# Kernel tuning notes

Hardware: AMD Instinct MI355X
Metric: run time of the kernel (lower is better)

Reference implementation:

```python
import jax, jax.numpy as jnp
from jax import lax
import numpy as np

EPS = 1e-5  # BatchNorm eps (eval mode, fresh running stats: mean=0, var=1)

N, T, H, C = 16, 512, 64, 64
O, K, E = 64, 9, 256


def setup_inputs() -> dict:
    key = jax.random.key(0)
    ks = jax.random.split(key, 16)
    X = jax.random.normal(ks[0], (N, T, H, C), dtype=jnp.float32)
    edges = jax.random.randint(ks[1], (N, 2, E), 0, H, dtype=jnp.int64)
    # att1/att2: Conv2d(C,1,1) == dot over channels + bias
    w_att1 = jax.random.normal(ks[2], (C,), jnp.float32) * (1.0 / np.sqrt(C))
    b_att1 = jax.random.normal(ks[3], (), jnp.float32) * 0.01
    w_att2 = jax.random.normal(ks[4], (C,), jnp.float32) * (1.0 / np.sqrt(C))
    b_att2 = jax.random.normal(ks[5], (), jnp.float32) * 0.01
    # GCN linear
    W_lin = jax.random.normal(ks[6], (O, C), jnp.float32) * (1.0 / np.sqrt(C))
    b_lin = jax.random.normal(ks[7], (O,), jnp.float32) * 0.01
    # tcn: BN -> ReLU -> Conv2d(O,O,(K,1)) -> BN -> Dropout(eval=id)
    bn1_gamma = 1.0 + 0.1 * jax.random.normal(ks[8], (O,), jnp.float32)
    bn1_beta = 0.1 * jax.random.normal(ks[9], (O,), jnp.float32)
    W_tcn = jax.random.normal(ks[10], (O, O, K, 1), jnp.float32) * (1.0 / np.sqrt(O * K))
    b_tcn = jax.random.normal(ks[11], (O,), jnp.float32) * 0.01
    bn2_gamma = 1.0 + 0.1 * jax.random.normal(ks[12], (O,), jnp.float32)
    bn2_beta = 0.1 * jax.random.normal(ks[13], (O,), jnp.float32)
    return dict(X=X, edges=edges, w_att1=w_att1, b_att1=b_att1, w_att2=w_att2,
                b_att2=b_att2, W_lin=W_lin, b_lin=b_lin, bn1_gamma=bn1_gamma,
                bn1_beta=bn1_beta, W_tcn=W_tcn, b_tcn=b_tcn,
                bn2_gamma=bn2_gamma, bn2_beta=bn2_beta)


def _bn_eval(x, gamma, beta):
    # eval-mode BatchNorm2d with running_mean=0, running_var=1; x is (N, Cc, T, H)
    inv = gamma / jnp.sqrt(1.0 + EPS)
    return x * inv[None, :, None, None] + beta[None, :, None, None]


def _forward(X, edges, w_att1, b_att1, w_att2, b_att2, W_lin, b_lin,
             bn1_gamma, bn1_beta, W_tcn, b_tcn, bn2_gamma, bn2_beta):
    n, t, h, c = X.shape
    k = W_tcn.shape[2]
    # --- adjacency from edge lists (duplicates sum, as sparse_coo->to_dense) ---
    bidx = jnp.arange(n)[:, None]
    adj = jnp.zeros((n, h, h), X.dtype).at[bidx, edges[:, 0, :], edges[:, 1, :]].add(1.0)
    # --- attention: a1[n,t,h] + a2[n,t,h'], leaky_relu, softmax over h ---
    a1 = jnp.einsum('nthc,c->nth', X, w_att1) + b_att1
    a2 = jnp.einsum('nthc,c->nth', X, w_att2) + b_att2
    s = jax.nn.leaky_relu(a1[:, :, :, None] + a2[:, :, None, :], 0.01)  # (n,t,h,h')
    att = jax.nn.softmax(s, axis=2)  # softmax over h (dim=1 pre-permute)
    # --- GCN: einsum('nthh,ntho->ntho') only uses diag(adj@att + I) ---
    diag = jnp.einsum('nhk,ntkh->nth', adj, att) + 1.0
    support = jnp.einsum('nthc,oc->ntho', X, W_lin) + b_lin  # (n,t,h,O)
    g = diag[..., None] * support
    # --- tcn: BN -> ReLU -> temporal conv (K,1) -> BN -> Dropout(eval) ---
    y = jnp.transpose(g, (0, 3, 1, 2))  # (n,O,t,h)
    y = jax.nn.relu(_bn_eval(y, bn1_gamma, bn1_beta))
    pad = (k - 1) // 2
    y = lax.conv_general_dilated(y, W_tcn, window_strides=(1, 1),
                                 padding=[(pad, pad), (0, 0)])
    y = y + b_tcn[None, :, None, None]
    y = _bn_eval(y, bn2_gamma, bn2_beta)
    # --- residual (identity: in==out, stride=1) + relu ---
    y = y + jnp.transpose(X, (0, 3, 1, 2))
    return jnp.transpose(jax.nn.relu(y), (0, 2, 3, 1))  # (n,t,h,O)


def reference(X, edges, w_att1, b_att1, w_att2, b_att2, W_lin, b_lin,
              bn1_gamma, bn1_beta, W_tcn, b_tcn, bn2_gamma, bn2_beta):
    return _forward(X, edges, w_att1, b_att1, w_att2, b_att2, W_lin, b_lin,
                    bn1_gamma, bn1_beta, W_tcn, b_tcn, bn2_gamma, bn2_beta)
```

## Files before the change

kernel.cpp:

```cpp
#include <hip/hip_runtime.h>
#include <hip/hip_bf16.h>
#include <stdint.h>

typedef float f32x4 __attribute__((ext_vector_type(4)));
typedef __bf16 bf16x8 __attribute__((ext_vector_type(8)));
typedef unsigned short u16;
typedef unsigned int u32;

__device__ __forceinline__ u16 f2bf(float f) {
    u32 u = __float_as_uint(f);
    u32 r = (u + 0x7fffu + ((u >> 16) & 1u)) >> 16;
    return (u16)r;
}

__global__ __launch_bounds__(256) void k_adj(const int* __restrict__ edges,
                                             float* __restrict__ adj) {
    __shared__ float a[64 * 64];
    const int n = blockIdx.x;
    for (int i = threadIdx.x; i < 4096; i += 256) a[i] = 0.f;
    __syncthreads();
    {
        int r = edges[n * 512 + threadIdx.x];
        int c = edges[n * 512 + 256 + threadIdx.x];
        atomicAdd(&a[r * 64 + c], 1.0f);
    }
    __syncthreads();
    for (int i = threadIdx.x; i < 4096; i += 256) adj[n * 4096 + i] = a[i];
}

__global__ __launch_bounds__(256) void k_pack(const float* __restrict__ Wlin,
                                              const float* __restrict__ Wtcn,
                                              u16* __restrict__ wlin_p,
                                              u16* __restrict__ wtcn_p) {
    int idx = blockIdx.x * 256 + threadIdx.x;
    if (idx < 4096) {
        int jj = idx & 7, l = (idx >> 3) & 63, j = (idx >> 9) & 3, s = idx >> 11;
        int o = j * 16 + (l & 15);
        int c = s * 32 + (l >> 4) * 8 + jj;
        wlin_p[idx] = f2bf(Wlin[o * 64 + c]);
    }
    int i2 = idx - 4096;
    if (i2 >= 0 && i2 < 36864) {
        int jj = i2 & 7, l = (i2 >> 3) & 63, j = (i2 >> 9) & 3, s = (i2 >> 11) & 1, kk = i2 >> 12;
        int o = j * 16 + (l & 15);
        int op = s * 32 + (l >> 4) * 8 + jj;
        wtcn_p[i2] = f2bf(Wtcn[(o * 64 + op) * 9 + kk]);
    }
}

__global__ __launch_bounds__(256) void k_attn(
    const float* __restrict__ X, const float* __restrict__ adj,
    const float* __restrict__ w1g, const float* __restrict__ b1g,
    const float* __restrict__ w2g, const float* __restrict__ b2g,
    float* __restrict__ diag) {
    __shared__ float adjs[64 * 65];
    __shared__ float p1[64 * 17], p2[64 * 17];
    __shared__ float A1[64], A2[64];

    const int tid = threadIdx.x;
    const int n = blockIdx.x >> 9, t = blockIdx.x & 511;
    const float* Xrow = X + (size_t)(n * 512 + t) * 4096;

    {
        const int c4 = tid & 15;
        const int r0 = tid >> 4;
        float4 wv1 = *(const float4*)(w1g + c4 * 4);
        float4 wv2 = *(const float4*)(w2g + c4 * 4);
#pragma unroll
        for (int i = 0; i < 4; i++) {
            int h = r0 + 16 * i;
            float4 xv = *(const float4*)(Xrow + h * 64 + c4 * 4);
            p1[h * 17 + c4] = xv.x * wv1.x + xv.y * wv1.y + xv.z * wv1.z + xv.w * wv1.w;
            p2[h * 17 + c4] = xv.x * wv2.x + xv.y * wv2.y + xv.z * wv2.z + xv.w * wv2.w;
        }
        const float* adjn = adj + n * 4096;
#pragma unroll
        for (int i = 0; i < 16; i++) {
            int idx = tid + 256 * i;
            adjs[(idx >> 6) * 65 + (idx & 63)] = adjn[idx];
        }
    }
    __syncthreads();

    if (tid < 64) {
        float s = 0.f;
#pragma unroll
        for (int i = 0; i < 16; i++) s += p1[tid * 17 + i];
        A1[tid] = s + b1g[0];
    } else if (tid < 128) {
        int h = tid - 64;
        float s = 0.f;
#pragma unroll
        for (int i = 0; i < 16; i++) s += p2[h * 17 + i];
        A2[h] = s + b2g[0];
    }
    __syncthreads();

    {
        int h = tid >> 2, p = tid & 3;
        float a2h = A2[h];
        float num = 0.f, den = 0.f;
#pragma unroll
        for (int i = 0; i < 16; i++) {
            int k = p * 16 + i;
            float sv = A1[k] + a2h;
            sv = sv > 0.f ? sv : 0.01f * sv;
            float e = __expf(sv);
            den += e;
            num += adjs[h * 65 + k] * e;
        }
        p1[h * 17 + p] = num;
        p2[h * 17 + p] = den;
    }
    __syncthreads();
    if (tid < 64) {
        float num = p1[tid * 17 + 0] + p1[tid * 17 + 1] + p1[tid * 17 + 2] + p1[tid * 17 + 3];
        float den = p2[tid * 17 + 0] + p2[tid * 17 + 1] + p2[tid * 17 + 2] + p2[tid * 17 + 3];
        diag[((size_t)(n * 64 + tid)) * 512 + t] = num / den + 1.0f;
    }
}

__global__ __launch_bounds__(256) void k_gcn_tcn(
    const float* __restrict__ X, const float* __restrict__ diag,
    const u16* __restrict__ wlin_p, const float* __restrict__ blin,
    const float* __restrict__ g1, const float* __restrict__ be1,
    const u16* __restrict__ wtcn_p, const float* __restrict__ btcn,
    const float* __restrict__ g2, const float* __restrict__ be2,
    float* __restrict__ out) {
    __shared__ __align__(16) u16 As[144 * 72];
    __shared__ float DGs[144];

    const int tid = threadIdx.x;
    const int bid = blockIdx.x;
    const int n = bid >> 8, h = (bid >> 2) & 63, tb = (bid & 3) * 128;
    const float* Xbase = X + ((size_t)(n * 512) * 64 + h) * 64;

#pragma unroll
    for (int i = 0; i < 9; i++) {
        int idx = tid + 256 * i;
        int r = idx >> 4, c4 = idx & 15;
        int tg = tb - 4 + r;
        float4 xv = make_float4(0.f, 0.f, 0.f, 0.f);
        if (tg >= 0 && tg < 512) xv = *(const float4*)(Xbase + (size_t)tg * 4096 + c4 * 4);
        uint2 pk;
        pk.x = (u32)f2bf(xv.x) | ((u32)f2bf(xv.y) << 16);
        pk.y = (u32)f2bf(xv.z) | ((u32)f2bf(xv.w) << 16);
        *(uint2*)(&As[r * 72 + c4 * 4]) = pk;
    }
    if (tid < 144) {
        int tg = tb - 4 + tid;
        DGs[tid] = (tg >= 0 && tg < 512) ? diag[((size_t)(n * 64 + h)) * 512 + tg] : 0.f;
    }
    __syncthreads();

    const int w = tid >> 6, l = tid & 63;
    const int col = l & 15, q = l >> 4;
    const float rsf = 1.0f / sqrtf(1.0f + 1e-5f);
    const f32x4 zv = {0.f, 0.f, 0.f, 0.f};

    for (int mt = w; mt < 9; mt += 4) {
        f32x4 acc[4] = {zv, zv, zv, zv};
#pragma unroll
        for (int s = 0; s < 2; s++) {
            bf16x8 a = *(const bf16x8*)(&As[(16 * mt + col) * 72 + s * 32 + q * 8]);
#pragma unroll
            for (int j = 0; j < 4; j++) {
                bf16x8 b = *(const bf16x8*)(&wlin_p[((s * 4 + j) * 64 + l) * 8]);
                acc[j] = __builtin_amdgcn_mfma_f32_16x16x32_bf16(a, b, acc[j], 0, 0, 0);
            }
        }
#pragma unroll
        for (int j = 0; j < 4; j++) {
            int o = 16 * j + col;
            float s1 = g1[o] * rsf;
            float bb = be1[o];
            float bl = blin[o];
#pragma unroll
            for (int rr = 0; rr < 4; rr++) {
                int row = 16 * mt + q * 4 + rr;
                int tg = tb - 4 + row;
                float v = (acc[j][rr] + bl) * DGs[row] * s1 + bb;
                v = v > 0.f ? v : 0.f;
                if (tg < 0 || tg >= 512) v = 0.f;
                As[row * 72 + o] = f2bf(v);
            }
        }
    }
    __syncthreads();

    f32x4 acc2[2][4];
#pragma unroll
    for (int mt = 0; mt < 2; mt++)
#pragma unroll
        for (int j = 0; j < 4; j++) acc2[mt][j] = zv;

    for (int kk = 0; kk < 9; kk++) {
#pragma unroll
        for (int s = 0; s < 2; s++) {
            bf16x8 b[4];
#pragma unroll
            for (int j = 0; j < 4; j++)
                b[j] = *(const bf16x8*)(&wtcn_p[(((kk * 2 + s) * 4 + j) * 64 + l) * 8]);
            bf16x8 a[2];
#pragma unroll
            for (int mt = 0; mt < 2; mt++) {
                int row = 32 * w + 16 * mt + col + kk;
                a[mt] = *(const bf16x8*)(&As[row * 72 + s * 32 + q * 8]);
            }
#pragma unroll
            for (int mt = 0; mt < 2; mt++)
#pragma unroll
                for (int j = 0; j < 4; j++)
                    acc2[mt][j] = __builtin_amdgcn_mfma_f32_16x16x32_bf16(a[mt], b[j], acc2[mt][j], 0, 0, 0);
        }
    }

    float s2[4], c2[4];
#pragma unroll
    for (int j = 0; j < 4; j++) {
        int o = 16 * j + col;
        float s = g2[o] * rsf;
        s2[j] = s;
        c2[j] = btcn[o] * s + be2[o];
    }
#pragma unroll
    for (int mt = 0; mt < 2; mt++) {
#pragma unroll
        for (int rr = 0; rr < 4; rr++) {
            int tt = tb + 32 * w + 16 * mt + 4 * q + rr;
#pragma unroll
            for (int j = 0; j < 4; j++) {
                int o = 16 * j + col;
                size_t off = ((size_t)(n * 512 + tt) * 64 + h) * 64 + o;
                float v = acc2[mt][j][rr] * s2[j] + c2[j] + X[off];
                out[off] = v > 0.f ? v : 0.f;
            }
        }
    }
}

extern "C" void kernel_launch(void* const* d_in, const int* in_sizes, int n_in,
                              void* d_out, int out_size, void* d_ws, size_t ws_size,
                              hipStream_t stream) {
    const float* X    = (const float*)d_in[0];
    const int*  edges = (const int*)d_in[1];
    const float* w1   = (const float*)d_in[2];
    const float* b1   = (const float*)d_in[3];
    const float* w2   = (const float*)d_in[4];
    const float* b2   = (const float*)d_in[5];
    const float* Wlin = (const float*)d_in[6];
    const float* blin = (const float*)d_in[7];
    const float* g1   = (const float*)d_in[8];
    const float* be1  = (const float*)d_in[9];
    const float* Wtcn = (const float*)d_in[10];
    const float* btcn = (const float*)d_in[11];
    const float* g2   = (const float*)d_in[12];
    const float* be2  = (const float*)d_in[13];
    float* out = (float*)d_out;

    char* ws = (char*)d_ws;
    float* adj    = (float*)ws;
    u16*   wlin_p = (u16*)(ws + 262144);
    u16*   wtcn_p = (u16*)(ws + 262144 + 8192);
    float* diag   = (float*)(ws + 262144 + 8192 + 73728);

    hipLaunchKernelGGL(k_adj, dim3(16), dim3(256), 0, stream, edges, adj);
    hipLaunchKernelGGL(k_pack, dim3(160), dim3(256), 0, stream, Wlin, Wtcn, wlin_p, wtcn_p);
    hipLaunchKernelGGL(k_attn, dim3(16 * 512), dim3(256), 0, stream,
                       X, adj, w1, b1, w2, b2, diag);
    hipLaunchKernelGGL(k_gcn_tcn, dim3(16 * 64 * 4), dim3(256), 0, stream,
                       X, diag, wlin_p, blin, g1, be1, wtcn_p, btcn, g2, be2, out);
}
```

Before: 319.7 us.

## Retile GCN-TCN kernel over 8 timesteps by 32 nodes with swizzled LDS

The fused GCN+TCN kernel previously tiled one graph node over 128 timesteps, which needed strided global reads with a 4-row halo on each side (144 rows per 128 outputs). It now tiles 8 timesteps by 32 nodes, so global loads read contiguous runs of node rows. LDS uses an XOR chunk swizzle instead of padding to avoid bank conflicts, and diag is stored t-major to match. In exchange the halo overhead rises to 16 rows per 8 timesteps, so the first GEMM and the X loads do more redundant work, and the 64KB LDS tile may limit occupancy.

```diff
diff --git a/kernel.cpp b/kernel.cpp
--- a/kernel.cpp
+++ b/kernel.cpp
@@ -116,7 +116,7 @@
     if (tid < 64) {
         float num = p1[tid * 17 + 0] + p1[tid * 17 + 1] + p1[tid * 17 + 2] + p1[tid * 17 + 3];
         float den = p2[tid * 17 + 0] + p2[tid * 17 + 1] + p2[tid * 17 + 2] + p2[tid * 17 + 3];
-        diag[((size_t)(n * 64 + tid)) * 512 + t] = num / den + 1.0f;
+        diag[((size_t)(n * 512 + t)) * 64 + tid] = num / den + 1.0f;
     }
 }
 
@@ -127,48 +127,62 @@
     const u16* __restrict__ wtcn_p, const float* __restrict__ btcn,
     const float* __restrict__ g2, const float* __restrict__ be2,
     float* __restrict__ out) {
-    __shared__ __align__(16) u16 As[144 * 72];
-    __shared__ float DGs[144];
+    __shared__ __align__(16) u16 As[512 * 64];
+    __shared__ float DGs[512];
 
     const int tid = threadIdx.x;
     const int bid = blockIdx.x;
-    const int n = bid >> 8, h = (bid >> 2) & 63, tb = (bid & 3) * 128;
-    const float* Xbase = X + ((size_t)(n * 512) * 64 + h) * 64;
-
-#pragma unroll
-    for (int i = 0; i < 9; i++) {
-        int idx = tid + 256 * i;
-        int r = idx >> 4, c4 = idx & 15;
-        int tg = tb - 4 + r;
+    const int hh0 = (bid & 1) * 32;
+    const int t0 = ((bid >> 1) & 63) * 8;
+    const int n = bid >> 7;
+
+    const float* Xb = X + (((size_t)n * 512) * 64 + hh0) * 64;
+#pragma unroll 4
+    for (int i = 0; i < 32; i++) {
+        int idx = i * 256 + tid;
+        int ar = idx >> 4, c4 = idx & 15;
+        int tl = ar >> 5, hh = ar & 31;
+        int tg = t0 - 4 + tl;
         float4 xv = make_float4(0.f, 0.f, 0.f, 0.f);
-        if (tg >= 0 && tg < 512) xv = *(const float4*)(Xbase + (size_t)tg * 4096 + c4 * 4);
+        if (tg >= 0 && tg < 512)
+            xv = *(const float4*)(Xb + ((size_t)tg * 64 + hh) * 64 + c4 * 4);
         uint2 pk;
         pk.x = (u32)f2bf(xv.x) | ((u32)f2bf(xv.y) << 16);
         pk.y = (u32)f2bf(xv.z) | ((u32)f2bf(xv.w) << 16);
-        *(uint2*)(&As[r * 72 + c4 * 4]) = pk;
-    }
-    if (tid < 144) {
-        int tg = tb - 4 + tid;
-        DGs[tid] = (tg >= 0 && tg < 512) ? diag[((size_t)(n * 64 + h)) * 512 + tg] : 0.f;
+        int chunk = (c4 >> 1) ^ (ar & 7);
+        *(uint2*)(&As[ar * 64 + chunk * 8 + (c4 & 1) * 4]) = pk;
+    }
+#pragma unroll
+    for (int i = 0; i < 2; i++) {
+        int r = tid + 256 * i;
+        int tl = r >> 5, hh = r & 31;
+        int tg = t0 - 4 + tl;
+        DGs[r] = (tg >= 0 && tg < 512) ? diag[((size_t)(n * 512 + tg)) * 64 + hh0 + hh] : 0.f;
     }
     __syncthreads();
 
     const int w = tid >> 6, l = tid & 63;
     const int col = l & 15, q = l >> 4;
     const float rsf = 1.0f / sqrtf(1.0f + 1e-5f);
-    const f32x4 zv = {0.f, 0.f, 0.f, 0.f};
-
-    for (int mt = w; mt < 9; mt += 4) {
-        f32x4 acc[4] = {zv, zv, zv, zv};
+    const f32x4 zv4 = {0.f, 0.f, 0.f, 0.f};
+
+#pragma unroll
+    for (int i = 0; i < 8; i++) {
+        int st = w + 4 * i;
+        int rowbase = (st >> 1) * 32 + (st & 1) * 16;
+        int arow = rowbase + col;
+        f32x4 acc[4] = {zv4, zv4, zv4, zv4};
 #pragma unroll
         for (int s = 0; s < 2; s++) {
-            bf16x8 a = *(const bf16x8*)(&As[(16 * mt + col) * 72 + s * 32 + q * 8]);
+            bf16x8 a = *(const bf16x8*)(&As[arow * 64 + ((4 * s + q) ^ (arow & 7)) * 8]);
 #pragma unroll
             for (int j = 0; j < 4; j++) {
                 bf16x8 b = *(const bf16x8*)(&wlin_p[((s * 4 + j) * 64 + l) * 8]);
                 acc[j] = __builtin_amdgcn_mfma_f32_16x16x32_bf16(a, b, acc[j], 0, 0, 0);
             }
         }
+        int tg = t0 - 4 + (st >> 1);
+        bool live = (tg >= 0 && tg < 512);
 #pragma unroll
         for (int j = 0; j < 4; j++) {
             int o = 16 * j + col;
@@ -177,22 +191,20 @@
             float bl = blin[o];
 #pragma unroll
             for (int rr = 0; rr < 4; rr++) {
-                int row = 16 * mt + q * 4 + rr;
-                int tg = tb - 4 + row;
-                float v = (acc[j][rr] + bl) * DGs[row] * s1 + bb;
-                v = v > 0.f ? v : 0.f;
-                if (tg < 0 || tg >= 512) v = 0.f;
-                As[row * 72 + o] = f2bf(v);
-            }
-        }
-    }
-    __syncthreads();
-
-    f32x4 acc2[2][4];
-#pragma unroll
-    for (int mt = 0; mt < 2; mt++)
-#pragma unroll
-        for (int j = 0; j < 4; j++) acc2[mt][j] = zv;
+                int rm = rowbase + q * 4 + rr;
+                float v = (acc[j][rr] + bl) * DGs[rm] * s1 + bb;
+                v = (v > 0.f && live) ? v : 0.f;
+                As[rm * 64 + ((o >> 3) ^ (rm & 7)) * 8 + (o & 7)] = f2bf(v);
+            }
+        }
+    }
+    __syncthreads();
+
+    f32x4 acc2[4][4];
+#pragma unroll
+    for (int i = 0; i < 4; i++)
+#pragma unroll
+        for (int j = 0; j < 4; j++) acc2[i][j] = zv4;
 
     for (int kk = 0; kk < 9; kk++) {
 #pragma unroll
@@ -201,17 +213,15 @@
 #pragma unroll
             for (int j = 0; j < 4; j++)
                 b[j] = *(const bf16x8*)(&wtcn_p[(((kk * 2 + s) * 4 + j) * 64 + l) * 8]);
-            bf16x8 a[2];
-#pragma unroll
-            for (int mt = 0; mt < 2; mt++) {
-                int row = 32 * w + 16 * mt + col + kk;
-                a[mt] = *(const bf16x8*)(&As[row * 72 + s * 32 + q * 8]);
-            }
-#pragma unroll
-            for (int mt = 0; mt < 2; mt++)
+#pragma unroll
+            for (int i = 0; i < 4; i++) {
+                int ct = w + 4 * i;
+                int zr = ((ct >> 1) + kk) * 32 + (ct & 1) * 16 + col;
+                bf16x8 a = *(const bf16x8*)(&As[zr * 64 + ((4 * s + q) ^ (zr & 7)) * 8]);
 #pragma unroll
                 for (int j = 0; j < 4; j++)
-                    acc2[mt][j] = __builtin_amdgcn_mfma_f32_16x16x32_bf16(a[mt], b[j], acc2[mt][j], 0, 0, 0);
+                    acc2[i][j] = __builtin_amdgcn_mfma_f32_16x16x32_bf16(a, b[j], acc2[i][j], 0, 0, 0);
+            }
         }
     }
 
@@ -224,16 +234,20 @@
         c2[j] = btcn[o] * s + be2[o];
     }
 #pragma unroll
-    for (int mt = 0; mt < 2; mt++) {
+    for (int i = 0; i < 4; i++) {
+        int ct = w + 4 * i;
+        int t = t0 + (ct >> 1);
+        int hbase = hh0 + (ct & 1) * 16;
 #pragma unroll
         for (int rr = 0; rr < 4; rr++) {
-            int tt = tb + 32 * w + 16 * mt + 4 * q + rr;
+            int h = hbase + q * 4 + rr;
+            const float* Xr = X + (((size_t)(n * 512 + t)) * 64 + h) * 64;
+            float* Or = out + (((size_t)(n * 512 + t)) * 64 + h) * 64;
 #pragma unroll
             for (int j = 0; j < 4; j++) {
                 int o = 16 * j + col;
-                size_t off = ((size_t)(n * 512 + tt) * 64 + h) * 64 + o;
-                float v = acc2[mt][j][rr] * s2[j] + c2[j] + X[off];
-                out[off] = v > 0.f ? v : 0.f;
+                float v = acc2[i][j][rr] * s2[j] + c2[j] + Xr[o];
+                Or[o] = v > 0.f ? v : 0.f;
             }
         }
     }
@@ -268,6 +282,6 @@
     hipLaunchKernelGGL(k_pack, dim3(160), dim3(256), 0, stream, Wlin, Wtcn, wlin_p, wtcn_p);
     hipLaunchKernelGGL(k_attn, dim3(16 * 512), dim3(256), 0, stream,
                        X, adj, w1, b1, w2, b2, diag);
-    hipLaunchKernelGGL(k_gcn_tcn, dim3(16 * 64 * 4), dim3(256), 0, stream,
+    hipLaunchKernelGGL(k_gcn_tcn, dim3(16 * 64 * 2), dim3(256), 0, stream,
                        X, diag, wlin_p, blin, g1, be1, wtcn_p, btcn, g2, be2, out);
 }
```

Measured after the change: 369.2 us. 1.15x slower.

## Emit transposed bf16 X copy in attention pass and consume it in GCN-TCN

Applied to the files above, without the earlier changes.

The attention kernel now processes 8 timesteps per block and, while reading X once, writes a bf16 copy transposed to (n,h,t,c) with XOR-swizzled 16-byte chunks. The fused GCN/TCN kernel loads this compact contiguous copy with 16-byte loads instead of strided fp32 reads. It uses separate swizzled LDS buffers for X and the intermediate, and takes the residual from the bf16 tile instead of re-reading fp32 X from global memory. This lowers global traffic and uncoalesced access, at the cost of an extra 64 MB bf16 write, reduced residual precision, and a serial 64-iteration softmax loop per thread.

```diff
diff --git a/kernel.cpp b/kernel.cpp
--- a/kernel.cpp
+++ b/kernel.cpp
@@ -7,10 +7,9 @@
 typedef unsigned short u16;
 typedef unsigned int u32;
 
-__device__ __forceinline__ u16 f2bf(float f) {
+__device__ __forceinline__ u32 f2bf(float f) {
     u32 u = __float_as_uint(f);
-    u32 r = (u + 0x7fffu + ((u >> 16) & 1u)) >> 16;
-    return (u16)r;
+    return (u + 0x7fffu + ((u >> 16) & 1u)) >> 16;
 }
 
 __global__ __launch_bounds__(256) void k_adj(const int* __restrict__ edges,
@@ -37,115 +36,111 @@
         int jj = idx & 7, l = (idx >> 3) & 63, j = (idx >> 9) & 3, s = idx >> 11;
         int o = j * 16 + (l & 15);
         int c = s * 32 + (l >> 4) * 8 + jj;
-        wlin_p[idx] = f2bf(Wlin[o * 64 + c]);
+        wlin_p[idx] = (u16)f2bf(Wlin[o * 64 + c]);
     }
     int i2 = idx - 4096;
     if (i2 >= 0 && i2 < 36864) {
         int jj = i2 & 7, l = (i2 >> 3) & 63, j = (i2 >> 9) & 3, s = (i2 >> 11) & 1, kk = i2 >> 12;
         int o = j * 16 + (l & 15);
         int op = s * 32 + (l >> 4) * 8 + jj;
-        wtcn_p[i2] = f2bf(Wtcn[(o * 64 + op) * 9 + kk]);
-    }
-}
-
-__global__ __launch_bounds__(256) void k_attn(
+        wtcn_p[i2] = (u16)f2bf(Wtcn[(o * 64 + op) * 9 + kk]);
+    }
+}
+
+__global__ __launch_bounds__(256) void k_front(
     const float* __restrict__ X, const float* __restrict__ adj,
     const float* __restrict__ w1g, const float* __restrict__ b1g,
     const float* __restrict__ w2g, const float* __restrict__ b2g,
-    float* __restrict__ diag) {
+    u16* __restrict__ Xbf, float* __restrict__ diag) {
     __shared__ float adjs[64 * 65];
-    __shared__ float p1[64 * 17], p2[64 * 17];
-    __shared__ float A1[64], A2[64];
+    __shared__ float A1s[8 * 64], A2s[8 * 64];
 
     const int tid = threadIdx.x;
-    const int n = blockIdx.x >> 9, t = blockIdx.x & 511;
-    const float* Xrow = X + (size_t)(n * 512 + t) * 4096;
-
-    {
-        const int c4 = tid & 15;
-        const int r0 = tid >> 4;
-        float4 wv1 = *(const float4*)(w1g + c4 * 4);
-        float4 wv2 = *(const float4*)(w2g + c4 * 4);
-#pragma unroll
-        for (int i = 0; i < 4; i++) {
-            int h = r0 + 16 * i;
-            float4 xv = *(const float4*)(Xrow + h * 64 + c4 * 4);
-            p1[h * 17 + c4] = xv.x * wv1.x + xv.y * wv1.y + xv.z * wv1.z + xv.w * wv1.w;
-            p2[h * 17 + c4] = xv.x * wv2.x + xv.y * wv2.y + xv.z * wv2.z + xv.w * wv2.w;
-        }
-        const float* adjn = adj + n * 4096;
-#pragma unroll
-        for (int i = 0; i < 16; i++) {
-            int idx = tid + 256 * i;
-            adjs[(idx >> 6) * 65 + (idx & 63)] = adjn[idx];
-        }
-    }
-    __syncthreads();
-
-    if (tid < 64) {
-        float s = 0.f;
-#pragma unroll
-        for (int i = 0; i < 16; i++) s += p1[tid * 17 + i];
-        A1[tid] = s + b1g[0];
-    } else if (tid < 128) {
-        int h = tid - 64;
-        float s = 0.f;
-#pragma unroll
-        for (int i = 0; i < 16; i++) s += p2[h * 17 + i];
-        A2[h] = s + b2g[0];
-    }
-    __syncthreads();
-
-    {
-        int h = tid >> 2, p = tid & 3;
-        float a2h = A2[h];
+    const int n = blockIdx.x >> 6, t0 = (blockIdx.x & 63) * 8;
+
+    const float* adjn = adj + n * 4096;
+#pragma unroll
+    for (int i = 0; i < 16; i++) {
+        int idx = tid + 256 * i;
+        adjs[(idx >> 6) * 65 + (idx & 63)] = adjn[idx];
+    }
+
+    const int c4 = tid & 15, hb = tid >> 4;
+    float4 wv1 = *(const float4*)(w1g + c4 * 4);
+    float4 wv2 = *(const float4*)(w2g + c4 * 4);
+    const float b1 = b1g[0], b2 = b2g[0];
+
+    for (int tl = 0; tl < 8; tl++) {
+        int t = t0 + tl;
+        const float* Xt = X + ((size_t)(n * 512 + t)) * 4096;
+        int key = (t + 4) & 7;
+#pragma unroll
+        for (int p = 0; p < 4; p++) {
+            int h = hb + 16 * p;
+            float4 xv = *(const float4*)(Xt + h * 64 + c4 * 4);
+            float s1 = xv.x * wv1.x + xv.y * wv1.y + xv.z * wv1.z + xv.w * wv1.w;
+            float s2 = xv.x * wv2.x + xv.y * wv2.y + xv.z * wv2.z + xv.w * wv2.w;
+#pragma unroll
+            for (int m = 1; m < 16; m <<= 1) {
+                s1 += __shfl_xor(s1, m);
+                s2 += __shfl_xor(s2, m);
+            }
+            if (c4 == 0) {
+                A1s[tl * 64 + h] = s1 + b1;
+                A2s[tl * 64 + h] = s2 + b2;
+            }
+            uint2 pk;
+            pk.x = f2bf(xv.x) | (f2bf(xv.y) << 16);
+            pk.y = f2bf(xv.z) | (f2bf(xv.w) << 16);
+            int chunk = (c4 >> 1) ^ key;
+            *(uint2*)(Xbf + (((size_t)(n * 64 + h)) * 512 + t) * 64 + chunk * 8 + (c4 & 1) * 4) = pk;
+        }
+    }
+    __syncthreads();
+
+#pragma unroll
+    for (int pp = 0; pp < 2; pp++) {
+        int idx = tid + 256 * pp;
+        int tl = idx >> 6, h = idx & 63;
+        float a2h = A2s[tl * 64 + h];
         float num = 0.f, den = 0.f;
-#pragma unroll
-        for (int i = 0; i < 16; i++) {
-            int k = p * 16 + i;
-            float sv = A1[k] + a2h;
+        for (int k = 0; k < 64; k++) {
+            float sv = A1s[tl * 64 + k] + a2h;
             sv = sv > 0.f ? sv : 0.01f * sv;
             float e = __expf(sv);
             den += e;
             num += adjs[h * 65 + k] * e;
         }
-        p1[h * 17 + p] = num;
-        p2[h * 17 + p] = den;
-    }
-    __syncthreads();
-    if (tid < 64) {
-        float num = p1[tid * 17 + 0] + p1[tid * 17 + 1] + p1[tid * 17 + 2] + p1[tid * 17 + 3];
-        float den = p2[tid * 17 + 0] + p2[tid * 17 + 1] + p2[tid * 17 + 2] + p2[tid * 17 + 3];
-        diag[((size_t)(n * 64 + tid)) * 512 + t] = num / den + 1.0f;
+        diag[((size_t)(n * 64 + h)) * 512 + t0 + tl] = num / den + 1.0f;
     }
 }
 
 __global__ __launch_bounds__(256) void k_gcn_tcn(
-    const float* __restrict__ X, const float* __restrict__ diag,
+    const u16* __restrict__ Xbf, const float* __restrict__ diag,
     const u16* __restrict__ wlin_p, const float* __restrict__ blin,
     const float* __restrict__ g1, const float* __restrict__ be1,
     const u16* __restrict__ wtcn_p, const float* __restrict__ btcn,
     const float* __restrict__ g2, const float* __restrict__ be2,
     float* __restrict__ out) {
-    __shared__ __align__(16) u16 As[144 * 72];
+    __shared__ __align__(16) u16 As[144 * 64];
+    __shared__ __align__(16) u16 Zs[144 * 64];
     __shared__ float DGs[144];
 
     const int tid = threadIdx.x;
     const int bid = blockIdx.x;
     const int n = bid >> 8, h = (bid >> 2) & 63, tb = (bid & 3) * 128;
-    const float* Xbase = X + ((size_t)(n * 512) * 64 + h) * 64;
-
-#pragma unroll
-    for (int i = 0; i < 9; i++) {
-        int idx = tid + 256 * i;
-        int r = idx >> 4, c4 = idx & 15;
-        int tg = tb - 4 + r;
-        float4 xv = make_float4(0.f, 0.f, 0.f, 0.f);
-        if (tg >= 0 && tg < 512) xv = *(const float4*)(Xbase + (size_t)tg * 4096 + c4 * 4);
-        uint2 pk;
-        pk.x = (u32)f2bf(xv.x) | ((u32)f2bf(xv.y) << 16);
-        pk.y = (u32)f2bf(xv.z) | ((u32)f2bf(xv.w) << 16);
-        *(uint2*)(&As[r * 72 + c4 * 4]) = pk;
+    const u16* Xb = Xbf + (((size_t)(n * 64 + h)) * 512) * 64;
+
+#pragma unroll
+    for (int k = 0; k < 5; k++) {
+        int idx = tid + 256 * k;
+        if (idx < 1152) {
+            int r = idx >> 3, c = idx & 7;
+            int tg = tb - 4 + r;
+            tg = tg < 0 ? 0 : (tg > 511 ? 511 : tg);
+            uint4 v = *(const uint4*)(Xb + (size_t)tg * 64 + c * 8);
+            *(uint4*)(&As[r * 64 + c * 8]) = v;
+        }
     }
     if (tid < 144) {
         int tg = tb - 4 + tid;
@@ -156,13 +151,14 @@
     const int w = tid >> 6, l = tid & 63;
     const int col = l & 15, q = l >> 4;
     const float rsf = 1.0f / sqrtf(1.0f + 1e-5f);
-    const f32x4 zv = {0.f, 0.f, 0.f, 0.f};
-
-    for (int mt = w; mt < 9; mt += 4) {
-        f32x4 acc[4] = {zv, zv, zv, zv};
+    const f32x4 zv4 = {0.f, 0.f, 0.f, 0.f};
+
+    for (int st = w; st < 9; st += 4) {
+        int arow = 16 * st + col;
+        f32x4 acc[4] = {zv4, zv4, zv4, zv4};
 #pragma unroll
         for (int s = 0; s < 2; s++) {
-            bf16x8 a = *(const bf16x8*)(&As[(16 * mt + col) * 72 + s * 32 + q * 8]);
+            bf16x8 a = *(const bf16x8*)(&As[arow * 64 + (((4 * s + q) ^ (arow & 7)) * 8)]);
 #pragma unroll
             for (int j = 0; j < 4; j++) {
                 bf16x8 b = *(const bf16x8*)(&wlin_p[((s * 4 + j) * 64 + l) * 8]);
@@ -177,12 +173,11 @@
             float bl = blin[o];
 #pragma unroll
             for (int rr = 0; rr < 4; rr++) {
-                int row = 16 * mt + q * 4 + rr;
-                int tg = tb - 4 + row;
-                float v = (acc[j][rr] + bl) * DGs[row] * s1 + bb;
-                v = v > 0.f ? v : 0.f;
-                if (tg < 0 || tg >= 512) v = 0.f;
-                As[row * 72 + o] = f2bf(v);
+                int rm = 16 * st + q * 4 + rr;
+                int tg = tb - 4 + rm;
+                float v = (acc[j][rr] + bl) * DGs[rm] * s1 + bb;
+                v = (v > 0.f && tg >= 0 && tg < 512) ? v : 0.f;
+                Zs[rm * 64 + (((o >> 3) ^ (rm & 7)) * 8) + (o & 7)] = (u16)f2bf(v);
             }
         }
     }
@@ -190,9 +185,9 @@
 
     f32x4 acc2[2][4];
 #pragma unroll
-    for (int mt = 0; mt < 2; mt++)
-#pragma unroll
-        for (int j = 0; j < 4; j++) acc2[mt][j] = zv;
+    for (int i = 0; i < 2; i++)
+#pragma unroll
+        for (int j = 0; j < 4; j++) acc2[i][j] = zv4;
 
     for (int kk = 0; kk < 9; kk++) {
 #pragma unroll
@@ -201,17 +196,14 @@
 #pragma unroll
             for (int j = 0; j < 4; j++)
                 b[j] = *(const bf16x8*)(&wtcn_p[(((kk * 2 + s) * 4 + j) * 64 + l) * 8]);
-            bf16x8 a[2];
 #pragma unroll
             for (int mt = 0; mt < 2; mt++) {
-                int row = 32 * w + 16 * mt + col + kk;
-                a[mt] = *(const bf16x8*)(&As[row * 72 + s * 32 + q * 8]);
-            }
-#pragma unroll
-            for (int mt = 0; mt < 2; mt++)
+                int zr = 32 * w + 16 * mt + col + kk;
+                bf16x8 a = *(const bf16x8*)(&Zs[zr * 64 + (((4 * s + q) ^ (zr & 7)) * 8)]);
 #pragma unroll
                 for (int j = 0; j < 4; j++)
-                    acc2[mt][j] = __builtin_amdgcn_mfma_f32_16x16x32_bf16(a[mt], b[j], acc2[mt][j], 0, 0, 0);
+                    acc2[mt][j] = __builtin_amdgcn_mfma_f32_16x16x32_bf16(a, b[j], acc2[mt][j], 0, 0, 0);
+            }
         }
     }
 
@@ -227,13 +219,17 @@
     for (int mt = 0; mt < 2; mt++) {
 #pragma unroll
         for (int rr = 0; rr < 4; rr++) {
-            int tt = tb + 32 * w + 16 * mt + 4 * q + rr;
+            int lr = 32 * w + 16 * mt + 4 * q + rr;
+            int xrow = lr + 4;
+            int tt = tb + lr;
+            float* Or = out + (((size_t)(n * 512 + tt)) * 64 + h) * 64;
 #pragma unroll
             for (int j = 0; j < 4; j++) {
                 int o = 16 * j + col;
-                size_t off = ((size_t)(n * 512 + tt) * 64 + h) * 64 + o;
-                float v = acc2[mt][j][rr] * s2[j] + c2[j] + X[off];
-                out[off] = v > 0.f ? v : 0.f;
+                u16 xr = As[xrow * 64 + ((((o >> 3) ^ (xrow & 7)) * 8)) + (o & 7)];
+                float xres = __uint_as_float(((u32)xr) << 16);
+                float v = acc2[mt][j][rr] * s2[j] + c2[j] + xres;
+                Or[o] = v > 0.f ? v : 0.f;
             }
         }
     }
@@ -261,13 +257,14 @@
     char* ws = (char*)d_ws;
     float* adj    = (float*)ws;
     u16*   wlin_p = (u16*)(ws + 262144);
-    u16*   wtcn_p = (u16*)(ws + 262144 + 8192);
-    float* diag   = (float*)(ws + 262144 + 8192 + 73728);
+    u16*   wtcn_p = (u16*)(ws + 270336);
+    float* diag   = (float*)(ws + 344064);
+    u16*   Xbf    = (u16*)(ws + 344064 + 2097152);
 
     hipLaunchKernelGGL(k_adj, dim3(16), dim3(256), 0, stream, edges, adj);
     hipLaunchKernelGGL(k_pack, dim3(160), dim3(256), 0, stream, Wlin, Wtcn, wlin_p, wtcn_p);
-    hipLaunchKernelGGL(k_attn, dim3(16 * 512), dim3(256), 0, stream,
-                       X, adj, w1, b1, w2, b2, diag);
+    hipLaunchKernelGGL(k_front, dim3(16 * 64), dim3(256), 0, stream,
+                       X, adj, w1, b1, w2, b2, Xbf, diag);
     hipLaunchKernelGGL(k_gcn_tcn, dim3(16 * 64 * 4), dim3(256), 0, stream,
-                       X, diag, wlin_p, blin, g1, be1, wtcn_p, btcn, g2, be2, out);
-}
+                       Xbf, diag, wlin_p, blin, g1, be1, wtcn_p, btcn, g2, be2, out);
+}
```

New measurement: 355.2 us. +11.1%, slower.
